# Kernel tuning notes

Hardware: AMD Instinct MI355X
Metric: run time of the kernel (lower is better)

The kernel has to match this reference:

```python
import jax, jax.numpy as jnp
import numpy as np

B, NDET, NT, NY, NX = 4, 128, 2048, 256, 256
D, L, NH, PS = 256, 6, 8, 16
HP, WP = NY // PS, NX // PS
N = HP * WP


def setup_inputs() -> dict:
    key = jax.random.key(0)
    ks = jax.random.split(key, 12)
    w = lambda k, s: jax.random.normal(k, s, jnp.float32) * 0.02
    sino = jax.random.normal(ks[0], (B, 1, NDET, NT), jnp.float32)
    # LUT: channel 0 = floor temporal index (float, some out-of-range -> masked), channel 1 = interp alpha
    kf = jax.random.randint(ks[1], (NY, NX, NDET), -8, NT).astype(jnp.float32)
    alpha = jax.random.uniform(ks[2], (NY, NX, NDET), dtype=jnp.float32)
    lut = jnp.stack([kf, alpha], axis=-1)
    return {
        "sino": sino, "lut": lut,
        "patch_w": w(ks[3], (D, PS * PS)), "patch_b": jnp.zeros((D,), jnp.float32),
        "pos_embed": w(ks[4], (1, N, D)),
        "ln1_g": jnp.ones((L, D), jnp.float32), "ln1_b": jnp.zeros((L, D), jnp.float32),
        "wqkv": w(ks[5], (L, 3 * D, D)), "bqkv": jnp.zeros((L, 3 * D), jnp.float32),
        "wo": w(ks[6], (L, D, D)), "bo": jnp.zeros((L, D), jnp.float32),
        "ln2_g": jnp.ones((L, D), jnp.float32), "ln2_b": jnp.zeros((L, D), jnp.float32),
        "w1": w(ks[7], (L, 4 * D, D)), "b1": jnp.zeros((L, 4 * D), jnp.float32),
        "w2": w(ks[8], (L, D, 4 * D)), "b2": jnp.zeros((L, D), jnp.float32),
        "proj_w": w(ks[9], (PS * PS, D)), "proj_b": jnp.zeros((PS * PS,), jnp.float32),
        "conv_w": w(ks[10], (1, 1, 3, 3)), "conv_b": jnp.zeros((1,), jnp.float32),
    }


def _layernorm(x, g, b):
    m = x.mean(-1, keepdims=True)
    v = x.var(-1, keepdims=True)
    return (x - m) / jnp.sqrt(v + 1e-5) * g + b


def _mha(x, wqkv, bqkv, wo, bo):
    Bq, Nt, Dd = x.shape
    hd = Dd // NH
    qkv = x @ wqkv.T + bqkv                       # [B,N,3D]
    q, k, v = jnp.split(qkv, 3, axis=-1)
    sp = lambda t: t.reshape(Bq, Nt, NH, hd).transpose(0, 2, 1, 3)  # [B,H,N,hd]
    q, k, v = sp(q), sp(k), sp(v)
    scores = jnp.einsum('bhnd,bhmd->bhnm', q, k) / jnp.sqrt(jnp.float32(hd))
    att = jax.nn.softmax(scores, axis=-1)
    o = jnp.einsum('bhnm,bhmd->bhnd', att, v).transpose(0, 2, 1, 3).reshape(Bq, Nt, Dd)
    return o @ wo.T + bo


def _backproject(sino, lut):
    # sino: [B,1,n_det,n_t]; lut: [ny,nx,n_det,2] -> image [B,1,ny,nx]
    n_t = sino.shape[-1]
    kf = lut[..., 0].astype(jnp.int32)
    alpha = lut[..., 1]
    valid = (kf >= 0) & (kf < n_t - 1)
    k0 = jnp.clip(kf, 0, n_t - 2)
    k1 = k0 + 1
    S = sino[:, 0]                                # [B, n_det, n_t]
    d_idx = jnp.arange(NDET)[None, None, :]       # broadcast over (ny, nx)

    def per_batch(Sb):                            # Sb: [n_det, n_t]
        s0 = Sb[d_idx, k0]                        # [ny,nx,n_det]
        s1 = Sb[d_idx, k1]
        sk = (1.0 - alpha) * s0 + alpha * s1
        return jnp.where(valid, sk, 0.0)

    sk = jax.vmap(per_batch)(S)                   # [B,ny,nx,n_det]
    apod = 0.5 - 0.5 * jnp.cos(2.0 * jnp.pi * jnp.arange(NDET) / (NDET - 1))
    apod = apod.astype(sino.dtype)
    out = jnp.einsum('byxd,d->byx', sk, apod) / jnp.maximum(apod.sum(), 1e-6)
    return out[:, None]                           # [B,1,ny,nx]


def reference(sino, lut, patch_w, patch_b, pos_embed, ln1_g, ln1_b, wqkv, bqkv,
              wo, bo, ln2_g, ln2_b, w1, b1, w2, b2, proj_w, proj_b, conv_w, conv_b):
    bp_img = _backproject(sino, lut)              # [B,1,NY,NX]
    # patch embed (Conv2d k=stride=patch  ==  patch-flatten + linear)
    x = bp_img[:, 0].reshape(B, HP, PS, WP, PS).transpose(0, 1, 3, 2, 4).reshape(B, N, PS * PS)
    z = x @ patch_w.T + patch_b                   # [B,N,D]
    z = z + pos_embed
    for l in range(L):
        y = _layernorm(z, ln1_g[l], ln1_b[l])
        z = z + _mha(y, wqkv[l], bqkv[l], wo[l], bo[l])
        y = _layernorm(z, ln2_g[l], ln2_b[l])
        y = jax.nn.gelu(y @ w1[l].T + b1[l], approximate=False) @ w2[l].T + b2[l]
        z = z + y
    pixels = z @ proj_w.T + proj_b                # [B,N,PS*PS]
    pixels = pixels.reshape(B, HP, WP, PS, PS).transpose(0, 1, 3, 2, 4)
    img = pixels.reshape(B, 1, HP * PS, WP * PS)
    img = jax.lax.conv_general_dilated(img, conv_w, (1, 1), 'SAME',
                                       dimension_numbers=('NCHW', 'OIHW', 'NCHW'))
    img = img + conv_b.reshape(1, 1, 1, 1)
    img = img + bp_img                            # residual (shapes match)
    return (img, bp_img)
```

## Files before the change

kernel.cpp:

```cpp
#include <hip/hip_runtime.h>
#include <hip/hip_bf16.h>
#include <math.h>

#define BB 4
#define NDET 128
#define NT 2048
#define DD 256
#define LL 6
#define MROWS 1024

typedef __attribute__((ext_vector_type(8))) short s8v;
typedef __attribute__((ext_vector_type(4))) float f32x4;
typedef unsigned short ushort_t;

__device__ __forceinline__ unsigned short f2b(float x) {
  union { float f; unsigned u; } v; v.f = x;
  unsigned r = v.u + 0x7fff + ((v.u >> 16) & 1);
  return (unsigned short)(r >> 16);
}
__device__ __forceinline__ unsigned pk2(float a, float b) {
  return (unsigned)f2b(a) | ((unsigned)f2b(b) << 16);
}
__device__ __forceinline__ float gelu_exact(float x) {
  return 0.5f * x * (1.0f + erff(x * 0.70710678118654752f));
}

__global__ __launch_bounds__(256) void cast_all(
    const float* __restrict__ s0, const float* __restrict__ s1,
    const float* __restrict__ s2, const float* __restrict__ s3,
    const float* __restrict__ s4, const float* __restrict__ s5,
    unsigned short* __restrict__ d0, unsigned short* __restrict__ d1,
    unsigned short* __restrict__ d2, unsigned short* __restrict__ d3,
    unsigned short* __restrict__ d4, unsigned short* __restrict__ d5)
{
  const int e0 = 16384, e1 = 311296, e2 = 409600, e3 = 802816, e4 = 1196032,
            e5 = 1212416;
  int i = blockIdx.x * 256 + threadIdx.x;
  int stride = gridDim.x * 256;
  for (; i < e5; i += stride) {
    const float* s; unsigned short* d; int j;
    if (i < e0)      { s = s0; d = d0; j = i; }
    else if (i < e1) { s = s1; d = d1; j = i - e0; }
    else if (i < e2) { s = s2; d = d2; j = i - e1; }
    else if (i < e3) { s = s3; d = d3; j = i - e2; }
    else if (i < e4) { s = s4; d = d4; j = i - e3; }
    else             { s = s5; d = d5; j = i - e4; }
    float4 f = ((const float4*)s)[j];
    uint2 uv;
    uv.x = pk2(f.x, f.y);
    uv.y = pk2(f.z, f.w);
    ((uint2*)d)[j] = uv;
  }
}

__global__ __launch_bounds__(256) void bp_part(
    const float* __restrict__ sino, const float* __restrict__ lut,
    float* __restrict__ partial)
{
  __shared__ float apod[NDET];
  int tid = threadIdx.x;
  if (tid < NDET) {
    float ap = 0.5f - 0.5f * cosf(6.283185307179586f * (float)tid / 127.0f);
    apod[tid] = ap * (1.0f / 63.5f);
  }
  __syncthreads();
  int c = blockIdx.x >> 8;
  int pb = blockIdx.x & 255;
  int pix = pb * 256 + tid;
  const float* lrow = lut + (size_t)pix * 256;
  float acc[4] = {0.f, 0.f, 0.f, 0.f};
#pragma unroll
  for (int d0 = c * 16; d0 < c * 16 + 16; d0 += 4) {
    float4 l0 = *(const float4*)(lrow + d0 * 2);
    float4 l1 = *(const float4*)(lrow + d0 * 2 + 4);
    float kfs[4] = {l0.x, l0.z, l1.x, l1.z};
    float als[4] = {l0.y, l0.w, l1.y, l1.w};
#pragma unroll
    for (int dd = 0; dd < 4; ++dd) {
      int kf = (int)kfs[dd];
      if (kf >= 0 && kf < NT - 1) {
        float al = als[dd];
        float ap = apod[d0 + dd];
        float w0 = (1.0f - al) * ap, w1 = al * ap;
        const float* srow = sino + (d0 + dd) * NT + kf;
#pragma unroll
        for (int b = 0; b < 4; ++b)
          acc[b] += w0 * srow[b * NDET * NT] + w1 * srow[b * NDET * NT + 1];
      }
    }
  }
#pragma unroll
  for (int b = 0; b < 4; ++b)
    partial[(size_t)(c * 4 + b) * 65536 + pix] = acc[b];
}

__global__ __launch_bounds__(256) void bp_reduce(
    const float* __restrict__ partial, float* __restrict__ bp,
    float* __restrict__ out_bp)
{
  int pix = blockIdx.x * 256 + threadIdx.x;
#pragma unroll
  for (int b = 0; b < 4; ++b) {
    float s = 0.f;
#pragma unroll
    for (int c = 0; c < 8; ++c) s += partial[(size_t)(c * 4 + b) * 65536 + pix];
    bp[b * 65536 + pix] = s;
    out_bp[b * 65536 + pix] = s;
  }
}

template<int ACT, int RES, int AMODE, int OMODE>
__global__ __launch_bounds__(256) void gemm2(
    const float* __restrict__ A, const unsigned short* __restrict__ Wb,
    const float* __restrict__ bias, const float* __restrict__ res,
    const float* __restrict__ lng, const float* __restrict__ lnb,
    float* __restrict__ C, unsigned short* __restrict__ C16,
    int M, int N, int K, int res_mask)
{
  __shared__ __align__(16) unsigned short As[32][264];
  __shared__ __align__(16) unsigned short Bs[64][264];
  int bm = blockIdx.y * 32, bn = blockIdx.x * 64;
  int tid = threadIdx.x;
  int lane = tid & 63, w = tid >> 6;
  int lr = lane & 15, hi = lane >> 4;
  int lk = hi * 8, lg = hi * 4;
  int wr = (w & 1) * 16, wc = (w >> 1) * 32;
  f32x4 acc[2];
  acc[0] = (f32x4){0.f, 0.f, 0.f, 0.f};
  acc[1] = (f32x4){0.f, 0.f, 0.f, 0.f};

  for (int kc = 0; kc < K; kc += 256) {
    if (kc) __syncthreads();
    if (AMODE == 2) {
      float4 gl = ((const float4*)lng)[lane];
      float4 bl = ((const float4*)lnb)[lane];
#pragma unroll
      for (int rr = 0; rr < 8; ++rr) {
        int row = w * 8 + rr;
        float4 v = ((const float4*)(A + (size_t)(bm + row) * 256))[lane];
        float s = v.x + v.y + v.z + v.w;
#pragma unroll
        for (int off = 32; off; off >>= 1) s += __shfl_xor(s, off);
        float mean = s * (1.0f / 256.0f);
        float q = (v.x - mean) * (v.x - mean) + (v.y - mean) * (v.y - mean) +
                  (v.z - mean) * (v.z - mean) + (v.w - mean) * (v.w - mean);
#pragma unroll
        for (int off = 32; off; off >>= 1) q += __shfl_xor(q, off);
        float inv = 1.0f / sqrtf(q * (1.0f / 256.0f) + 1e-5f);
        float y0 = (v.x - mean) * inv * gl.x + bl.x;
        float y1 = (v.y - mean) * inv * gl.y + bl.y;
        float y2 = (v.z - mean) * inv * gl.z + bl.z;
        float y3 = (v.w - mean) * inv * gl.w + bl.w;
        uint2 u2; u2.x = pk2(y0, y1); u2.y = pk2(y2, y3);
        *(uint2*)&As[row][lane * 4] = u2;
      }
    } else {
      int r = tid >> 3, cbase = (tid & 7) * 32;
#pragma unroll
      for (int q8 = 0; q8 < 8; ++q8) {
        int k = cbase + q8 * 4;
        float4 f;
        if (AMODE == 0) {
          f = *(const float4*)(A + (size_t)(bm + r) * K + kc + k);
        } else {
          int m = bm + r;
          int bb = m >> 8, nn = m & 255;
          int ii = k >> 4, jj = k & 15;
          f = *(const float4*)(A + (size_t)bb * 65536 +
                               ((nn >> 4) * 16 + ii) * 256 + (nn & 15) * 16 + jj);
        }
        uint2 u2; u2.x = pk2(f.x, f.y); u2.y = pk2(f.z, f.w);
        *(uint2*)&As[r][k] = u2;
      }
    }
    {
      int r = tid >> 2, cbase = (tid & 3) * 64;
      const unsigned short* wp = Wb + (size_t)(bn + r) * K + kc + cbase;
#pragma unroll
      for (int q8 = 0; q8 < 8; ++q8)
        *(uint4*)&Bs[r][cbase + q8 * 8] = *(const uint4*)(wp + q8 * 8);
    }
    __syncthreads();
#pragma unroll
    for (int k0 = 0; k0 < 256; k0 += 32) {
      s8v a = *(const s8v*)&As[wr + lr][k0 + lk];
      s8v b0 = *(const s8v*)&Bs[wc + lr][k0 + lk];
      s8v b1 = *(const s8v*)&Bs[wc + 16 + lr][k0 + lk];
      acc[0] = __builtin_amdgcn_mfma_f32_16x16x32_bf16(a, b0, acc[0], 0, 0, 0);
      acc[1] = __builtin_amdgcn_mfma_f32_16x16x32_bf16(a, b1, acc[1], 0, 0, 0);
    }
  }

#pragma unroll
  for (int j = 0; j < 2; ++j) {
    int n = bn + wc + j * 16 + lr;
    float bv = bias[n];
#pragma unroll
    for (int r4 = 0; r4 < 4; ++r4) {
      int m = bm + wr + lg + r4;
      float c = acc[j][r4] + bv;
      if (ACT == 1) c = gelu_exact(c);
      if (RES == 1) c += res[(size_t)(m & res_mask) * N + n];
      if (OMODE == 0) {
        C[(size_t)m * N + n] = c;
      } else if (OMODE == 1) {
        int bb = m >> 8, t2 = m & 255;
        C[(size_t)bb * 65536 + ((t2 >> 4) * 16 + (n >> 4)) * 256 +
          (t2 & 15) * 16 + (n & 15)] = c;
      } else {
        C16[(size_t)m * N + n] = f2b(c);
      }
    }
  }
}

__global__ __launch_bounds__(256) void attn_fused(
    const unsigned short* __restrict__ qkv, float* __restrict__ o)
{
  __shared__ __align__(16) unsigned short Kl[256][40];
  __shared__ __align__(16) unsigned short Qb[32][40];
  __shared__ __align__(16) unsigned short Vt[32][264];
  __shared__ __align__(16) unsigned short Pl[32][264];
  __shared__ __align__(16) float Sf[32][268];
  int bi = blockIdx.x;
  int qc = bi & 7, h = (bi >> 3) & 7, b = bi >> 6;
  int tid = threadIdx.x, lane = tid & 63, w = tid >> 6;
  int lr = lane & 15, hi = lane >> 4;
  int lk = hi * 8, lg = hi * 4;
  const unsigned short* base = qkv + (size_t)b * 256 * 768;

  {
    const unsigned short* kr = base + tid * 768 + 256 + h * 32;
#pragma unroll
    for (int cq = 0; cq < 4; ++cq)
      *(uint4*)&Kl[tid][cq * 8] = *(const uint4*)(kr + cq * 8);
    const unsigned short* vr = base + tid * 768 + 512 + h * 32;
    unsigned short tmp[32];
#pragma unroll
    for (int cq = 0; cq < 4; ++cq)
      *(uint4*)&tmp[cq * 8] = *(const uint4*)(vr + cq * 8);
#pragma unroll
    for (int cc = 0; cc < 32; ++cc) Vt[cc][tid] = tmp[cc];
    int row = tid >> 3, c0 = (tid & 7) * 4;
    *(uint2*)&Qb[row][c0] =
        *(const uint2*)(base + (qc * 32 + row) * 768 + h * 32 + c0);
  }
  __syncthreads();

  {
    s8v qa0 = *(const s8v*)&Qb[lr][lk];
    s8v qa1 = *(const s8v*)&Qb[16 + lr][lk];
    f32x4 z4 = (f32x4){0.f, 0.f, 0.f, 0.f};
#pragma unroll
    for (int j = 0; j < 4; ++j) {
      s8v kb = *(const s8v*)&Kl[w * 64 + j * 16 + lr][lk];
      f32x4 s0 = __builtin_amdgcn_mfma_f32_16x16x32_bf16(qa0, kb, z4, 0, 0, 0);
      f32x4 s1 = __builtin_amdgcn_mfma_f32_16x16x32_bf16(qa1, kb, z4, 0, 0, 0);
#pragma unroll
      for (int r4 = 0; r4 < 4; ++r4) {
        Sf[lg + r4][w * 64 + j * 16 + lr] = s0[r4];
        Sf[16 + lg + r4][w * 64 + j * 16 + lr] = s1[r4];
      }
    }
  }
  __syncthreads();

  {
    const float scale = 0.17677669529663687f;
    for (int rr = 0; rr < 8; ++rr) {
      int row = w * 8 + rr;
      float4 v = *(const float4*)&Sf[row][lane * 4];
      v.x *= scale; v.y *= scale; v.z *= scale; v.w *= scale;
      float mx = fmaxf(fmaxf(v.x, v.y), fmaxf(v.z, v.w));
#pragma unroll
      for (int off = 32; off; off >>= 1) mx = fmaxf(mx, __shfl_xor(mx, off));
      float e0 = expf(v.x - mx), e1 = expf(v.y - mx);
      float e2 = expf(v.z - mx), e3 = expf(v.w - mx);
      float ss = e0 + e1 + e2 + e3;
#pragma unroll
      for (int off = 32; off; off >>= 1) ss += __shfl_xor(ss, off);
      float inv = 1.0f / ss;
      uint2 u2;
      u2.x = pk2(e0 * inv, e1 * inv);
      u2.y = pk2(e2 * inv, e3 * inv);
      *(uint2*)&Pl[row][lane * 4] = u2;
    }
  }
  __syncthreads();

  {
    int wr = (w & 1) * 16, wc = (w >> 1) * 16;
    f32x4 oa = (f32x4){0.f, 0.f, 0.f, 0.f};
#pragma unroll
    for (int ks = 0; ks < 8; ++ks) {
      s8v pa = *(const s8v*)&Pl[wr + lr][ks * 32 + lk];
      s8v vb = *(const s8v*)&Vt[wc + lr][ks * 32 + lk];
      oa = __builtin_amdgcn_mfma_f32_16x16x32_bf16(pa, vb, oa, 0, 0, 0);
    }
#pragma unroll
    for (int r4 = 0; r4 < 4; ++r4) {
      int row = qc * 32 + wr + lg + r4;
      o[((size_t)(b * 256) + row) * 256 + h * 32 + wc + lr] = oa[r4];
    }
  }
}

__global__ __launch_bounds__(256) void conv_kernel(
    const float* __restrict__ img, const float* __restrict__ cw,
    const float* __restrict__ cb, const float* __restrict__ bp,
    float* __restrict__ out_img)
{
  int gid = blockIdx.x * 256 + threadIdx.x;
  int b = gid >> 16, rem = gid & 65535;
  int y = rem >> 8, x = rem & 255;
  const float* ip = img + (size_t)b * 65536;
  float s = cb[0];
#pragma unroll
  for (int dy = -1; dy <= 1; ++dy)
#pragma unroll
    for (int dx = -1; dx <= 1; ++dx) {
      int yy = y + dy, xx = x + dx;
      if (yy >= 0 && yy < 256 && xx >= 0 && xx < 256)
        s += cw[(dy + 1) * 3 + (dx + 1)] * ip[yy * 256 + xx];
    }
  out_img[gid] = s + bp[gid];
}

extern "C" void kernel_launch(void* const* d_in, const int* in_sizes, int n_in,
                              void* d_out, int out_size, void* d_ws, size_t ws_size,
                              hipStream_t stream) {
  const float* sino    = (const float*)d_in[0];
  const float* lut     = (const float*)d_in[1];
  const float* patch_w = (const float*)d_in[2];
  const float* patch_b = (const float*)d_in[3];
  const float* pos     = (const float*)d_in[4];
  const float* ln1_g   = (const float*)d_in[5];
  const float* ln1_b   = (const float*)d_in[6];
  const float* wqkv    = (const float*)d_in[7];
  const float* bqkv    = (const float*)d_in[8];
  const float* wo      = (const float*)d_in[9];
  const float* bo      = (const float*)d_in[10];
  const float* ln2_g   = (const float*)d_in[11];
  const float* ln2_b   = (const float*)d_in[12];
  const float* w1      = (const float*)d_in[13];
  const float* b1      = (const float*)d_in[14];
  const float* w2      = (const float*)d_in[15];
  const float* b2      = (const float*)d_in[16];
  const float* proj_w  = (const float*)d_in[17];
  const float* proj_b  = (const float*)d_in[18];
  const float* conv_w  = (const float*)d_in[19];
  const float* conv_b  = (const float*)d_in[20];
  float* out = (float*)d_out;
  float* ws  = (float*)d_ws;

  float* bpb     = ws;
  float* z       = bpb + 262144;
  float* ob      = z + 262144;
  float* hb      = ob + 262144;
  float* imgp    = hb + 1048576;
  float* partial = imgp + 262144;
  unsigned short* wsu    = (unsigned short*)(partial + 2097152);
  unsigned short* pwb    = wsu;
  unsigned short* qkvw   = pwb + 65536;
  unsigned short* wow    = qkvw + 1179648;
  unsigned short* w1w    = wow + 393216;
  unsigned short* w2w    = w1w + 1572864;
  unsigned short* projw  = w2w + 1572864;
  unsigned short* qkvb16 = projw + 65536;

  cast_all<<<2048, 256, 0, stream>>>(patch_w, wqkv, wo, w1, w2, proj_w,
                                     pwb, qkvw, wow, w1w, w2w, projw);

  bp_part<<<2048, 256, 0, stream>>>(sino, lut, partial);
  bp_reduce<<<256, 256, 0, stream>>>(partial, bpb, out + 262144);

  gemm2<0, 1, 1, 0><<<dim3(4, 32), 256, 0, stream>>>(
      bpb, pwb, patch_b, pos, nullptr, nullptr, z, nullptr,
      MROWS, 256, 256, 255);

  for (int l = 0; l < LL; ++l) {
    gemm2<0, 0, 2, 2><<<dim3(12, 32), 256, 0, stream>>>(
        z, qkvw + (size_t)l * 196608, bqkv + l * 768, nullptr,
        ln1_g + l * 256, ln1_b + l * 256, nullptr, qkvb16,
        MROWS, 768, 256, 0);
    attn_fused<<<256, 256, 0, stream>>>(qkvb16, ob);
    gemm2<0, 1, 0, 0><<<dim3(4, 32), 256, 0, stream>>>(
        ob, wow + (size_t)l * 65536, bo + l * 256, z, nullptr, nullptr,
        z, nullptr, MROWS, 256, 256, 1023);
    gemm2<1, 0, 2, 0><<<dim3(16, 32), 256, 0, stream>>>(
        z, w1w + (size_t)l * 262144, b1 + l * 1024, nullptr,
        ln2_g + l * 256, ln2_b + l * 256, hb, nullptr,
        MROWS, 1024, 256, 0);
    gemm2<0, 1, 0, 0><<<dim3(4, 32), 256, 0, stream>>>(
        hb, w2w + (size_t)l * 262144, b2 + l * 256, z, nullptr, nullptr,
        z, nullptr, MROWS, 256, 1024, 1023);
  }

  gemm2<0, 0, 0, 1><<<dim3(4, 32), 256, 0, stream>>>(
      z, projw, proj_b, nullptr, nullptr, nullptr, imgp, nullptr,
      MROWS, 256, 256, 0);
  conv_kernel<<<1024, 256, 0, stream>>>(imgp, conv_w, conv_b, bpb, out);
}
```

Baseline: 522.8 us.

## Interleave sinogram batches, enlarge GEMM M-tile, keep attention/MLP intermediates in bf16

A new pre-pass interleaves the four batch sinograms so that each backprojection tap reads two float4 values instead of eight scattered scalars. The GEMM kernel's M tile grows from 32 to 64 rows, with a 2x2 MFMA accumulator per wave, which halves the number of blocks and doubles reuse of the weight tile. The attention output and the MLP hidden activations are now written as bf16 and loaded straight into shared memory by a new input mode, which skips the fp32 round-trip and the in-kernel conversion. The trade-offs are an extra transpose kernel with its own buffer, fewer blocks per GEMM, and rounding of the hidden activations that were previously fp32.

Result: slower. 548.7 us (+5.0%).

```diff
diff --git a/kernel.cpp b/kernel.cpp
--- a/kernel.cpp
+++ b/kernel.cpp
@@ -53,8 +53,20 @@
   }
 }
 
+__global__ __launch_bounds__(256) void transpose_sino(
+    const float* __restrict__ sino, float* __restrict__ st)
+{
+  int idx = blockIdx.x * 256 + threadIdx.x;
+  float4 v;
+  v.x = sino[idx];
+  v.y = sino[262144 + idx];
+  v.z = sino[524288 + idx];
+  v.w = sino[786432 + idx];
+  ((float4*)st)[idx] = v;
+}
+
 __global__ __launch_bounds__(256) void bp_part(
-    const float* __restrict__ sino, const float* __restrict__ lut,
+    const float* __restrict__ st, const float* __restrict__ lut,
     float* __restrict__ partial)
 {
   __shared__ float apod[NDET];
@@ -68,7 +80,8 @@
   int pb = blockIdx.x & 255;
   int pix = pb * 256 + tid;
   const float* lrow = lut + (size_t)pix * 256;
-  float acc[4] = {0.f, 0.f, 0.f, 0.f};
+  const float4* sp = (const float4*)st;
+  float a0 = 0.f, a1 = 0.f, a2 = 0.f, a3 = 0.f;
 #pragma unroll
   for (int d0 = c * 16; d0 < c * 16 + 16; d0 += 4) {
     float4 l0 = *(const float4*)(lrow + d0 * 2);
@@ -82,16 +95,19 @@
         float al = als[dd];
         float ap = apod[d0 + dd];
         float w0 = (1.0f - al) * ap, w1 = al * ap;
-        const float* srow = sino + (d0 + dd) * NT + kf;
-#pragma unroll
-        for (int b = 0; b < 4; ++b)
-          acc[b] += w0 * srow[b * NDET * NT] + w1 * srow[b * NDET * NT + 1];
+        const float4* q = sp + (d0 + dd) * NT + kf;
+        float4 s0 = q[0], s1 = q[1];
+        a0 += w0 * s0.x + w1 * s1.x;
+        a1 += w0 * s0.y + w1 * s1.y;
+        a2 += w0 * s0.z + w1 * s1.z;
+        a3 += w0 * s0.w + w1 * s1.w;
       }
     }
   }
-#pragma unroll
-  for (int b = 0; b < 4; ++b)
-    partial[(size_t)(c * 4 + b) * 65536 + pix] = acc[b];
+  partial[(size_t)(c * 4 + 0) * 65536 + pix] = a0;
+  partial[(size_t)(c * 4 + 1) * 65536 + pix] = a1;
+  partial[(size_t)(c * 4 + 2) * 65536 + pix] = a2;
+  partial[(size_t)(c * 4 + 3) * 65536 + pix] = a3;
 }
 
 __global__ __launch_bounds__(256) void bp_reduce(
@@ -110,24 +126,27 @@
 }
 
 template<int ACT, int RES, int AMODE, int OMODE>
-__global__ __launch_bounds__(256) void gemm2(
-    const float* __restrict__ A, const unsigned short* __restrict__ Wb,
+__global__ __launch_bounds__(256) void gemm3(
+    const float* __restrict__ A, const unsigned short* __restrict__ A16,
+    const unsigned short* __restrict__ Wb,
     const float* __restrict__ bias, const float* __restrict__ res,
     const float* __restrict__ lng, const float* __restrict__ lnb,
     float* __restrict__ C, unsigned short* __restrict__ C16,
     int M, int N, int K, int res_mask)
 {
-  __shared__ __align__(16) unsigned short As[32][264];
+  __shared__ __align__(16) unsigned short As[64][264];
   __shared__ __align__(16) unsigned short Bs[64][264];
-  int bm = blockIdx.y * 32, bn = blockIdx.x * 64;
+  int bm = blockIdx.y * 64, bn = blockIdx.x * 64;
   int tid = threadIdx.x;
   int lane = tid & 63, w = tid >> 6;
   int lr = lane & 15, hi = lane >> 4;
   int lk = hi * 8, lg = hi * 4;
-  int wr = (w & 1) * 16, wc = (w >> 1) * 32;
-  f32x4 acc[2];
-  acc[0] = (f32x4){0.f, 0.f, 0.f, 0.f};
-  acc[1] = (f32x4){0.f, 0.f, 0.f, 0.f};
+  int wr = (w & 1) * 32, wc = (w >> 1) * 32;
+  f32x4 acc[2][2];
+#pragma unroll
+  for (int i = 0; i < 2; ++i)
+#pragma unroll
+    for (int j = 0; j < 2; ++j) acc[i][j] = (f32x4){0.f, 0.f, 0.f, 0.f};
 
   for (int kc = 0; kc < K; kc += 256) {
     if (kc) __syncthreads();
@@ -135,8 +154,8 @@
       float4 gl = ((const float4*)lng)[lane];
       float4 bl = ((const float4*)lnb)[lane];
 #pragma unroll
-      for (int rr = 0; rr < 8; ++rr) {
-        int row = w * 8 + rr;
+      for (int rr = 0; rr < 16; ++rr) {
+        int row = w * 16 + rr;
         float4 v = ((const float4*)(A + (size_t)(bm + row) * 256))[lane];
         float s = v.x + v.y + v.z + v.w;
 #pragma unroll
@@ -154,68 +173,85 @@
         uint2 u2; u2.x = pk2(y0, y1); u2.y = pk2(y2, y3);
         *(uint2*)&As[row][lane * 4] = u2;
       }
+    } else if (AMODE == 3) {
+      int r = tid >> 2, cb = (tid & 3) * 64;
+      const unsigned short* ap = A16 + (size_t)(bm + r) * K + kc + cb;
+#pragma unroll
+      for (int q8 = 0; q8 < 8; ++q8)
+        *(uint4*)&As[r][cb + q8 * 8] = *(const uint4*)(ap + q8 * 8);
     } else {
-      int r = tid >> 3, cbase = (tid & 7) * 32;
+      int r = tid >> 2, cb = (tid & 3) * 64;
 #pragma unroll
       for (int q8 = 0; q8 < 8; ++q8) {
-        int k = cbase + q8 * 4;
-        float4 f;
+        int k = cb + q8 * 8;
+        float4 f0, f1;
         if (AMODE == 0) {
-          f = *(const float4*)(A + (size_t)(bm + r) * K + kc + k);
+          const float* ap = A + (size_t)(bm + r) * K + kc + k;
+          f0 = *(const float4*)ap;
+          f1 = *(const float4*)(ap + 4);
         } else {
           int m = bm + r;
           int bb = m >> 8, nn = m & 255;
-          int ii = k >> 4, jj = k & 15;
-          f = *(const float4*)(A + (size_t)bb * 65536 +
-                               ((nn >> 4) * 16 + ii) * 256 + (nn & 15) * 16 + jj);
+          int k1 = k, k2 = k + 4;
+          f0 = *(const float4*)(A + (size_t)bb * 65536 +
+               ((nn >> 4) * 16 + (k1 >> 4)) * 256 + (nn & 15) * 16 + (k1 & 15));
+          f1 = *(const float4*)(A + (size_t)bb * 65536 +
+               ((nn >> 4) * 16 + (k2 >> 4)) * 256 + (nn & 15) * 16 + (k2 & 15));
         }
-        uint2 u2; u2.x = pk2(f.x, f.y); u2.y = pk2(f.z, f.w);
-        *(uint2*)&As[r][k] = u2;
+        uint4 u;
+        u.x = pk2(f0.x, f0.y); u.y = pk2(f0.z, f0.w);
+        u.z = pk2(f1.x, f1.y); u.w = pk2(f1.z, f1.w);
+        *(uint4*)&As[r][k] = u;
       }
     }
     {
-      int r = tid >> 2, cbase = (tid & 3) * 64;
-      const unsigned short* wp = Wb + (size_t)(bn + r) * K + kc + cbase;
+      int r = tid >> 2, cb = (tid & 3) * 64;
+      const unsigned short* wp = Wb + (size_t)(bn + r) * K + kc + cb;
 #pragma unroll
       for (int q8 = 0; q8 < 8; ++q8)
-        *(uint4*)&Bs[r][cbase + q8 * 8] = *(const uint4*)(wp + q8 * 8);
+        *(uint4*)&Bs[r][cb + q8 * 8] = *(const uint4*)(wp + q8 * 8);
     }
     __syncthreads();
 #pragma unroll
     for (int k0 = 0; k0 < 256; k0 += 32) {
-      s8v a = *(const s8v*)&As[wr + lr][k0 + lk];
+      s8v a0 = *(const s8v*)&As[wr + lr][k0 + lk];
+      s8v a1 = *(const s8v*)&As[wr + 16 + lr][k0 + lk];
       s8v b0 = *(const s8v*)&Bs[wc + lr][k0 + lk];
       s8v b1 = *(const s8v*)&Bs[wc + 16 + lr][k0 + lk];
-      acc[0] = __builtin_amdgcn_mfma_f32_16x16x32_bf16(a, b0, acc[0], 0, 0, 0);
-      acc[1] = __builtin_amdgcn_mfma_f32_16x16x32_bf16(a, b1, acc[1], 0, 0, 0);
-    }
-  }
-
-#pragma unroll
-  for (int j = 0; j < 2; ++j) {
-    int n = bn + wc + j * 16 + lr;
-    float bv = bias[n];
-#pragma unroll
-    for (int r4 = 0; r4 < 4; ++r4) {
-      int m = bm + wr + lg + r4;
-      float c = acc[j][r4] + bv;
-      if (ACT == 1) c = gelu_exact(c);
-      if (RES == 1) c += res[(size_t)(m & res_mask) * N + n];
-      if (OMODE == 0) {
-        C[(size_t)m * N + n] = c;
-      } else if (OMODE == 1) {
-        int bb = m >> 8, t2 = m & 255;
-        C[(size_t)bb * 65536 + ((t2 >> 4) * 16 + (n >> 4)) * 256 +
-          (t2 & 15) * 16 + (n & 15)] = c;
-      } else {
-        C16[(size_t)m * N + n] = f2b(c);
+      acc[0][0] = __builtin_amdgcn_mfma_f32_16x16x32_bf16(a0, b0, acc[0][0], 0, 0, 0);
+      acc[0][1] = __builtin_amdgcn_mfma_f32_16x16x32_bf16(a0, b1, acc[0][1], 0, 0, 0);
+      acc[1][0] = __builtin_amdgcn_mfma_f32_16x16x32_bf16(a1, b0, acc[1][0], 0, 0, 0);
+      acc[1][1] = __builtin_amdgcn_mfma_f32_16x16x32_bf16(a1, b1, acc[1][1], 0, 0, 0);
+    }
+  }
+
+#pragma unroll
+  for (int i = 0; i < 2; ++i)
+#pragma unroll
+    for (int j = 0; j < 2; ++j) {
+      int n = bn + wc + j * 16 + lr;
+      float bv = bias[n];
+#pragma unroll
+      for (int r4 = 0; r4 < 4; ++r4) {
+        int m = bm + wr + i * 16 + lg + r4;
+        float c = acc[i][j][r4] + bv;
+        if (ACT == 1) c = gelu_exact(c);
+        if (RES == 1) c += res[(size_t)(m & res_mask) * N + n];
+        if (OMODE == 0) {
+          C[(size_t)m * N + n] = c;
+        } else if (OMODE == 1) {
+          int bb = m >> 8, t2 = m & 255;
+          C[(size_t)bb * 65536 + ((t2 >> 4) * 16 + (n >> 4)) * 256 +
+            (t2 & 15) * 16 + (n & 15)] = c;
+        } else {
+          C16[(size_t)m * N + n] = f2b(c);
+        }
       }
     }
-  }
 }
 
 __global__ __launch_bounds__(256) void attn_fused(
-    const unsigned short* __restrict__ qkv, float* __restrict__ o)
+    const unsigned short* __restrict__ qkv, unsigned short* __restrict__ o16)
 {
   __shared__ __align__(16) unsigned short Kl[256][40];
   __shared__ __align__(16) unsigned short Qb[32][40];
@@ -300,7 +336,7 @@
 #pragma unroll
     for (int r4 = 0; r4 < 4; ++r4) {
       int row = qc * 32 + wr + lg + r4;
-      o[((size_t)(b * 256) + row) * 256 + h * 32 + wc + lr] = oa[r4];
+      o16[((size_t)(b * 256) + row) * 256 + h * 32 + wc + lr] = f2b(oa[r4]);
     }
   }
 }
@@ -355,11 +391,10 @@
 
   float* bpb     = ws;
   float* z       = bpb + 262144;
-  float* ob      = z + 262144;
-  float* hb      = ob + 262144;
-  float* imgp    = hb + 1048576;
+  float* imgp    = z + 262144;
   float* partial = imgp + 262144;
-  unsigned short* wsu    = (unsigned short*)(partial + 2097152);
+  float* st      = partial + 2097152;
+  unsigned short* wsu    = (unsigned short*)(st + 1048576);
   unsigned short* pwb    = wsu;
   unsigned short* qkvw   = pwb + 65536;
   unsigned short* wow    = qkvw + 1179648;
@@ -367,37 +402,40 @@
   unsigned short* w2w    = w1w + 1572864;
   unsigned short* projw  = w2w + 1572864;
   unsigned short* qkvb16 = projw + 65536;
+  unsigned short* hb16   = qkvb16 + 786432;
+  unsigned short* ob16   = hb16 + 1048576;
 
   cast_all<<<2048, 256, 0, stream>>>(patch_w, wqkv, wo, w1, w2, proj_w,
                                      pwb, qkvw, wow, w1w, w2w, projw);
 
-  bp_part<<<2048, 256, 0, stream>>>(sino, lut, partial);
+  transpose_sino<<<1024, 256, 0, stream>>>(sino, st);
+  bp_part<<<2048, 256, 0, stream>>>(st, lut, partial);
   bp_reduce<<<256, 256, 0, stream>>>(partial, bpb, out + 262144);
 
-  gemm2<0, 1, 1, 0><<<dim3(4, 32), 256, 0, stream>>>(
-      bpb, pwb, patch_b, pos, nullptr, nullptr, z, nullptr,
+  gemm3<0, 1, 1, 0><<<dim3(4, 16), 256, 0, stream>>>(
+      bpb, nullptr, pwb, patch_b, pos, nullptr, nullptr, z, nullptr,
       MROWS, 256, 256, 255);
 
   for (int l = 0; l < LL; ++l) {
-    gemm2<0, 0, 2, 2><<<dim3(12, 32), 256, 0, stream>>>(
-        z, qkvw + (size_t)l * 196608, bqkv + l * 768, nullptr,
+    gemm3<0, 0, 2, 2><<<dim3(12, 16), 256, 0, stream>>>(
+        z, nullptr, qkvw + (size_t)l * 196608, bqkv + l * 768, nullptr,
         ln1_g + l * 256, ln1_b + l * 256, nullptr, qkvb16,
         MROWS, 768, 256, 0);
-    attn_fused<<<256, 256, 0, stream>>>(qkvb16, ob);
-    gemm2<0, 1, 0, 0><<<dim3(4, 32), 256, 0, stream>>>(
-        ob, wow + (size_t)l * 65536, bo + l * 256, z, nullptr, nullptr,
-        z, nullptr, MROWS, 256, 256, 1023);
-    gemm2<1, 0, 2, 0><<<dim3(16, 32), 256, 0, stream>>>(
-        z, w1w + (size_t)l * 262144, b1 + l * 1024, nullptr,
-        ln2_g + l * 256, ln2_b + l * 256, hb, nullptr,
+    attn_fused<<<256, 256, 0, stream>>>(qkvb16, ob16);
+    gemm3<0, 1, 3, 0><<<dim3(4, 16), 256, 0, stream>>>(
+        nullptr, ob16, wow + (size_t)l * 65536, bo + l * 256, z,
+        nullptr, nullptr, z, nullptr, MROWS, 256, 256, 1023);
+    gemm3<1, 0, 2, 2><<<dim3(16, 16), 256, 0, stream>>>(
+        z, nullptr, w1w + (size_t)l * 262144, b1 + l * 1024, nullptr,
+        ln2_g + l * 256, ln2_b + l * 256, nullptr, hb16,
         MROWS, 1024, 256, 0);
-    gemm2<0, 1, 0, 0><<<dim3(4, 32), 256, 0, stream>>>(
-        hb, w2w + (size_t)l * 262144, b2 + l * 256, z, nullptr, nullptr,
-        z, nullptr, MROWS, 256, 1024, 1023);
-  }
-
-  gemm2<0, 0, 0, 1><<<dim3(4, 32), 256, 0, stream>>>(
-      z, projw, proj_b, nullptr, nullptr, nullptr, imgp, nullptr,
+    gemm3<0, 1, 3, 0><<<dim3(4, 16), 256, 0, stream>>>(
+        nullptr, hb16, w2w + (size_t)l * 262144, b2 + l * 256, z,
+        nullptr, nullptr, z, nullptr, MROWS, 256, 1024, 1023);
+  }
+
+  gemm3<0, 0, 0, 1><<<dim3(4, 16), 256, 0, stream>>>(
+      z, nullptr, projw, proj_b, nullptr, nullptr, nullptr, imgp, nullptr,
       MROWS, 256, 256, 0);
   conv_kernel<<<1024, 256, 0, stream>>>(imgp, conv_w, conv_b, bpb, out);
 }
```
